# Performance work log

Measured on AMD Instinct MI355X. Metric: run time of the kernel, lower is better.

## Reference

```python
import jax, jax.numpy as jnp
import numpy as np

NEG_INF_DIAG = 1000000.0

def setup_inputs() -> dict:
    key = jax.random.key(0)
    k1, k2, k3 = jax.random.split(key, 3)
    B, N, S, D = 64, 32, 256, 128
    return {
        "query_embeddings": jax.random.normal(k1, (B, N, D), dtype=jnp.float32),
        "doc_embeddings": jax.random.normal(k2, (B, S, D), dtype=jnp.float32),
        "neg_doc_embeddings": jax.random.normal(k3, (B, S, D), dtype=jnp.float32),
    }

def _maxsim(q, d):
    # q: (b, n, dim), d: (b, s, dim) -> (b,) sum over n of max over s of q.d
    return jnp.einsum('bnd,bsd->bns', q, d).max(axis=2).sum(axis=1)

def reference(query_embeddings, doc_embeddings, neg_doc_embeddings):
    pos_scores = _maxsim(query_embeddings, doc_embeddings)
    neg_scores = _maxsim(query_embeddings, neg_doc_embeddings)
    loss = jax.nn.softplus(neg_scores - pos_scores).mean()

    # in-batch term: scores[b, c] = MaxSim(query b, doc c)
    scores = jnp.einsum('bnd,csd->bcns', query_embeddings, doc_embeddings).max(axis=3).sum(axis=2)  # (B, B)
    pos = jnp.diagonal(scores)
    B = scores.shape[0]
    neg = (scores - jnp.eye(B, dtype=scores.dtype) * NEG_INF_DIAG).max(axis=1)
    loss = loss + jax.nn.softplus(neg - pos).mean()
    return loss / 2
```

## Files before the change

### kernel.cpp

```cpp
#include <hip/hip_runtime.h>
#include <hip/hip_bf16.h>

#define B_SZ 64
#define N_Q 32

typedef __attribute__((ext_vector_type(8))) short bf16x8;
typedef __attribute__((ext_vector_type(4))) float f32x4;

static __device__ __forceinline__ unsigned short f2bf(float f) {
    __hip_bfloat16 h = __float2bfloat16(f);
    return *reinterpret_cast<unsigned short*>(&h);
}

static __device__ __forceinline__ bf16x8 cvt_frag(const float* __restrict__ src) {
    float4 a = reinterpret_cast<const float4*>(src)[0];
    float4 b = reinterpret_cast<const float4*>(src)[1];
    union { bf16x8 v; unsigned short u[8]; } t;
    t.u[0] = f2bf(a.x); t.u[1] = f2bf(a.y); t.u[2] = f2bf(a.z); t.u[3] = f2bf(a.w);
    t.u[4] = f2bf(b.x); t.u[5] = f2bf(b.y); t.u[6] = f2bf(b.z); t.u[7] = f2bf(b.w);
    return t.v;
}

#define MFMA(A, Bv, C) __builtin_amdgcn_mfma_f32_16x16x32_bf16(A, Bv, C, 0, 0, 0)

__global__ __launch_bounds__(256) void cvt_permute(const float* __restrict__ q,
                                                   const float* __restrict__ dd,
                                                   const float* __restrict__ nd,
                                                   unsigned short* __restrict__ DP,
                                                   unsigned short* __restrict__ QP) {
    const int blk = blockIdx.x, tid = threadIdx.x;
    if (blk < 2048) {
        const int o = blk * 256 + tid;
        const int doc = o >> 12;
        const int u = o & 4095;
        const int ln = u & 63, nt = (u >> 6) & 3, kk = (u >> 8) & 3, ch = u >> 10;
        const int s  = ch * 64 + nt * 16 + (ln & 15);
        const int k0 = kk * 32 + (ln >> 4) * 8;
        const float* src = ((doc < 64) ? (dd + (size_t)doc * 32768)
                                       : (nd + (size_t)(doc - 64) * 32768)) + s * 128 + k0;
        reinterpret_cast<bf16x8*>(DP)[o] = cvt_frag(src);
    } else {
        const int g = (blk - 2048) * 256 + tid;
        const int b = g >> 9, u = g & 511;
        const int ln = u & 63, mt = (u >> 6) & 1, kk = u >> 7;
        const int n  = mt * 16 + (ln & 15);
        const int k0 = kk * 32 + (ln >> 4) * 8;
        reinterpret_cast<bf16x8*>(QP)[g] = cvt_frag(q + (size_t)b * 4096 + n * 128 + k0);
    }
}

__global__ __launch_bounds__(256, 2) void maxsim_kernel(const unsigned short* __restrict__ QP,
                                                        const unsigned short* __restrict__ DP,
                                                        float* __restrict__ scores) {
    const int wg  = blockIdx.x;
    const int tid = threadIdx.x;
    const int wave = tid >> 6, lane = tid & 63;
    const int l15 = lane & 15;

    __shared__ bf16x8 docB[4096];
    __shared__ float wredN[4][4][8];

    const bf16x8* DP8 = reinterpret_cast<const bf16x8*>(DP);
    const bf16x8* QP8 = reinterpret_cast<const bf16x8*>(QP);

    int c, b;
    bool isNeg;
    if (wg < 1024) { c = wg >> 4; b = (wg & 15) * 4 + wave; isNeg = false; }
    else           { b = wg - 1024; c = b; isNeg = true; }
    const int dcc = isNeg ? (64 + b) : c;

    bf16x8 Af[4][2];
    const bf16x8* qsrc = QP8 + (size_t)b * 512 + lane;
    #pragma unroll
    for (int kk = 0; kk < 4; ++kk) {
        Af[kk][0] = qsrc[kk * 128];
        Af[kk][1] = qsrc[kk * 128 + 64];
    }

    const bf16x8* dsrc = DP8 + (size_t)dcc * 4096 + wave * 1024 + lane;
    #pragma unroll
    for (int f = 0; f < 16; ++f)
        docB[wave * 1024 + f * 64 + lane] = dsrc[f * 64];
    __syncthreads();

    float rmax[2][4];
    #pragma unroll
    for (int mt = 0; mt < 2; ++mt)
        #pragma unroll
        for (int r = 0; r < 4; ++r) rmax[mt][r] = -3.0e38f;

    const int nch = isNeg ? 1 : 4;
    for (int i = 0; i < nch; ++i) {
        const int ch = isNeg ? wave : ((wave + i) & 3);
        f32x4 acc[2][4] = {};
        #pragma unroll
        for (int kk = 0; kk < 4; ++kk) {
            #pragma unroll
            for (int nt = 0; nt < 4; ++nt) {
                bf16x8 Bv = docB[ch * 1024 + kk * 256 + nt * 64 + lane];
                acc[0][nt] = MFMA(Af[kk][0], Bv, acc[0][nt]);
                acc[1][nt] = MFMA(Af[kk][1], Bv, acc[1][nt]);
            }
        }
        #pragma unroll
        for (int mt = 0; mt < 2; ++mt)
            #pragma unroll
            for (int r = 0; r < 4; ++r)
                rmax[mt][r] = fmaxf(rmax[mt][r],
                    fmaxf(fmaxf(acc[mt][0][r], acc[mt][1][r]),
                          fmaxf(acc[mt][2][r], acc[mt][3][r])));
    }

    float part = 0.0f;
    #pragma unroll
    for (int mt = 0; mt < 2; ++mt)
        #pragma unroll
        for (int r = 0; r < 4; ++r) {
            float m = rmax[mt][r];
            m = fmaxf(m, __shfl_xor(m, 1, 64));
            m = fmaxf(m, __shfl_xor(m, 2, 64));
            m = fmaxf(m, __shfl_xor(m, 4, 64));
            m = fmaxf(m, __shfl_xor(m, 8, 64));
            if (isNeg) {
                if (l15 == 0) wredN[wave][lane >> 4][mt * 4 + r] = m;
            } else {
                part += m;
            }
        }
    if (!isNeg) {
        part += __shfl_xor(part, 16, 64);
        part += __shfl_xor(part, 32, 64);
        if (lane == 0) scores[(size_t)b * 65 + c] = part;
    } else {
        __syncthreads();
        if (tid < 32) {
            const int l4v = tid >> 3, slot = tid & 7;
            float m = fmaxf(fmaxf(wredN[0][l4v][slot], wredN[1][l4v][slot]),
                            fmaxf(wredN[2][l4v][slot], wredN[3][l4v][slot]));
            m += __shfl_xor(m, 1, 64);
            m += __shfl_xor(m, 2, 64);
            m += __shfl_xor(m, 4, 64);
            m += __shfl_xor(m, 8, 64);
            m += __shfl_xor(m, 16, 64);
            if (tid == 0) scores[(size_t)b * 65 + 64] = m;
        }
    }
}

static __device__ __forceinline__ float softplusf(float x) {
    return fmaxf(x, 0.0f) + log1pf(expf(-fabsf(x)));
}

__global__ __launch_bounds__(64) void loss_kernel(const float* __restrict__ scores,
                                                  float* __restrict__ out) {
    const int b = threadIdx.x;
    const float* row = scores + b * 65;
    const float pos  = row[b];
    const float negq = row[64];
    float nib = -1e30f;
    #pragma unroll
    for (int c = 0; c < B_SZ; ++c) {
        float v = row[c] - ((c == b) ? 1000000.0f : 0.0f);
        nib = fmaxf(nib, v);
    }
    float t = softplusf(negq - pos) + softplusf(nib - pos);
    t += __shfl_xor(t, 1, 64);
    t += __shfl_xor(t, 2, 64);
    t += __shfl_xor(t, 4, 64);
    t += __shfl_xor(t, 8, 64);
    t += __shfl_xor(t, 16, 64);
    t += __shfl_xor(t, 32, 64);
    if (b == 0) out[0] = t * (0.5f / 64.0f);
}

extern "C" void kernel_launch(void* const* d_in, const int* in_sizes, int n_in,
                              void* d_out, int out_size, void* d_ws, size_t ws_size,
                              hipStream_t stream) {
    const float* q  = (const float*)d_in[0];
    const float* dd = (const float*)d_in[1];
    const float* nd = (const float*)d_in[2];
    float* out = (float*)d_out;

    unsigned short* DP = (unsigned short*)d_ws;
    unsigned short* QP = DP + (size_t)128 * 32768;
    float* scores = (float*)(QP + (size_t)64 * 4096);

    cvt_permute<<<2176, 256, 0, stream>>>(q, dd, nd, DP, QP);

    maxsim_kernel<<<1024 + B_SZ, 256, 0, stream>>>(QP, DP, scores);

    loss_kernel<<<1, 64, 0, stream>>>(scores, out);
}
```

Before: 90.06 us.

## Fuse loss into maxsim via last-block atomic, use direct global-to-LDS loads

Drops the separate loss kernel launch: each maxsim workgroup bumps a global counter after a fence, and the last one to finish computes the softplus loss from the scores matrix. Document tiles are now loaded with global_load_lds so data goes straight into LDS without passing through registers, and the query fragment loads are issued after them. The workgroup-to-(b,c) mapping is also reordered to change which documents adjacent blocks share, for cache locality. This adds a device-wide atomic and fences, and relies on the counter being reset by the preceding conversion kernel.

```diff
diff --git a/kernel.cpp b/kernel.cpp
--- a/kernel.cpp
+++ b/kernel.cpp
@@ -3,6 +3,7 @@
 
 #define B_SZ 64
 #define N_Q 32
+#define TOTAL_WG 1088
 
 typedef __attribute__((ext_vector_type(8))) short bf16x8;
 typedef __attribute__((ext_vector_type(4))) float f32x4;
@@ -23,12 +24,25 @@
 
 #define MFMA(A, Bv, C) __builtin_amdgcn_mfma_f32_16x16x32_bf16(A, Bv, C, 0, 0, 0)
 
+static __device__ __forceinline__ void gload_lds16(const bf16x8* g, bf16x8* l) {
+    __builtin_amdgcn_global_load_lds(
+        (const __attribute__((address_space(1))) void*)g,
+        (__attribute__((address_space(3))) void*)l,
+        16, 0, 0);
+}
+
+static __device__ __forceinline__ float softplusf(float x) {
+    return fmaxf(x, 0.0f) + log1pf(expf(-fabsf(x)));
+}
+
 __global__ __launch_bounds__(256) void cvt_permute(const float* __restrict__ q,
                                                    const float* __restrict__ dd,
                                                    const float* __restrict__ nd,
                                                    unsigned short* __restrict__ DP,
-                                                   unsigned short* __restrict__ QP) {
+                                                   unsigned short* __restrict__ QP,
+                                                   unsigned int* __restrict__ cnt) {
     const int blk = blockIdx.x, tid = threadIdx.x;
+    if (blk == 0 && tid == 0) *cnt = 0u;
     if (blk < 2048) {
         const int o = blk * 256 + tid;
         const int doc = o >> 12;
@@ -51,7 +65,9 @@
 
 __global__ __launch_bounds__(256, 2) void maxsim_kernel(const unsigned short* __restrict__ QP,
                                                         const unsigned short* __restrict__ DP,
-                                                        float* __restrict__ scores) {
+                                                        float* __restrict__ scores,
+                                                        unsigned int* __restrict__ cnt,
+                                                        float* __restrict__ out) {
     const int wg  = blockIdx.x;
     const int tid = threadIdx.x;
     const int wave = tid >> 6, lane = tid & 63;
@@ -59,15 +75,27 @@
 
     __shared__ bf16x8 docB[4096];
     __shared__ float wredN[4][4][8];
+    __shared__ unsigned int lastBlk;
 
     const bf16x8* DP8 = reinterpret_cast<const bf16x8*>(DP);
     const bf16x8* QP8 = reinterpret_cast<const bf16x8*>(QP);
 
     int c, b;
     bool isNeg;
-    if (wg < 1024) { c = wg >> 4; b = (wg & 15) * 4 + wave; isNeg = false; }
-    else           { b = wg - 1024; c = b; isNeg = true; }
+    if (wg < 1024) {
+        const int x = wg & 7, i = wg >> 3;
+        c = x * 8 + (i & 7);
+        b = (i >> 3) * 4 + wave;
+        isNeg = false;
+    } else {
+        b = wg - 1024; c = b; isNeg = true;
+    }
     const int dcc = isNeg ? (64 + b) : c;
+
+    const bf16x8* dsrc = DP8 + (size_t)dcc * 4096 + wave * 1024 + lane;
+    #pragma unroll
+    for (int f = 0; f < 16; ++f)
+        gload_lds16(dsrc + f * 64, &docB[wave * 1024 + f * 64]);
 
     bf16x8 Af[4][2];
     const bf16x8* qsrc = QP8 + (size_t)b * 512 + lane;
@@ -76,11 +104,6 @@
         Af[kk][0] = qsrc[kk * 128];
         Af[kk][1] = qsrc[kk * 128 + 64];
     }
-
-    const bf16x8* dsrc = DP8 + (size_t)dcc * 4096 + wave * 1024 + lane;
-    #pragma unroll
-    for (int f = 0; f < 16; ++f)
-        docB[wave * 1024 + f * 64 + lane] = dsrc[f * 64];
     __syncthreads();
 
     float rmax[2][4];
@@ -145,32 +168,34 @@
             if (tid == 0) scores[(size_t)b * 65 + 64] = m;
         }
     }
-}
-
-static __device__ __forceinline__ float softplusf(float x) {
-    return fmaxf(x, 0.0f) + log1pf(expf(-fabsf(x)));
-}
-
-__global__ __launch_bounds__(64) void loss_kernel(const float* __restrict__ scores,
-                                                  float* __restrict__ out) {
-    const int b = threadIdx.x;
-    const float* row = scores + b * 65;
-    const float pos  = row[b];
-    const float negq = row[64];
-    float nib = -1e30f;
-    #pragma unroll
-    for (int c = 0; c < B_SZ; ++c) {
-        float v = row[c] - ((c == b) ? 1000000.0f : 0.0f);
-        nib = fmaxf(nib, v);
-    }
-    float t = softplusf(negq - pos) + softplusf(nib - pos);
-    t += __shfl_xor(t, 1, 64);
-    t += __shfl_xor(t, 2, 64);
-    t += __shfl_xor(t, 4, 64);
-    t += __shfl_xor(t, 8, 64);
-    t += __shfl_xor(t, 16, 64);
-    t += __shfl_xor(t, 32, 64);
-    if (b == 0) out[0] = t * (0.5f / 64.0f);
+
+    __threadfence();
+    __syncthreads();
+    if (tid == 0) lastBlk = (atomicAdd(cnt, 1u) == TOTAL_WG - 1u) ? 1u : 0u;
+    __syncthreads();
+    if (lastBlk != 0u) {
+        __threadfence();
+        if (tid < 64) {
+            const int bb = tid;
+            const float* row = scores + bb * 65;
+            const float pos  = row[bb];
+            const float negq = row[64];
+            float nib = -1e30f;
+            #pragma unroll
+            for (int cc = 0; cc < B_SZ; ++cc) {
+                float v = row[cc] - ((cc == bb) ? 1000000.0f : 0.0f);
+                nib = fmaxf(nib, v);
+            }
+            float t = softplusf(negq - pos) + softplusf(nib - pos);
+            t += __shfl_xor(t, 1, 64);
+            t += __shfl_xor(t, 2, 64);
+            t += __shfl_xor(t, 4, 64);
+            t += __shfl_xor(t, 8, 64);
+            t += __shfl_xor(t, 16, 64);
+            t += __shfl_xor(t, 32, 64);
+            if (bb == 0) out[0] = t * (0.5f / 64.0f);
+        }
+    }
 }
 
 extern "C" void kernel_launch(void* const* d_in, const int* in_sizes, int n_in,
@@ -184,10 +209,9 @@
     unsigned short* DP = (unsigned short*)d_ws;
     unsigned short* QP = DP + (size_t)128 * 32768;
     float* scores = (float*)(QP + (size_t)64 * 4096);
-
-    cvt_permute<<<2176, 256, 0, stream>>>(q, dd, nd, DP, QP);
-
-    maxsim_kernel<<<1024 + B_SZ, 256, 0, stream>>>(QP, DP, scores);
-
-    loss_kernel<<<1, 64, 0, stream>>>(scores, out);
-}
+    unsigned int* cnt = (unsigned int*)(scores + 65 * 64);
+
+    cvt_permute<<<2176, 256, 0, stream>>>(q, dd, nd, DP, QP, cnt);
+
+    maxsim_kernel<<<TOTAL_WG, 256, 0, stream>>>(QP, DP, scores, cnt, out);
+}
```

Measured after the change: 153.1 us. 1.7x slower.

## Fuse fp32-to-bf16 conversion into maxsim kernel and remap workgroups for L2 reuse

Applied to the files above, without the earlier changes.

Drops the separate cvt_permute kernel and its workspace. The maxsim kernel now reads fp32 query and doc embeddings directly and converts them to bf16 fragments while filling registers and LDS. This removes one kernel launch and the round trip through a bf16 staging buffer. In exchange, each doc is re-read and re-converted by the 16 workgroups that use it. The workgroup-to-(doc, query group) mapping is also changed so that concurrently scheduled groups spread across docs, which may improve cache locality.

```diff
diff --git a/kernel.cpp b/kernel.cpp
--- a/kernel.cpp
+++ b/kernel.cpp
@@ -23,64 +23,49 @@
 
 #define MFMA(A, Bv, C) __builtin_amdgcn_mfma_f32_16x16x32_bf16(A, Bv, C, 0, 0, 0)
 
-__global__ __launch_bounds__(256) void cvt_permute(const float* __restrict__ q,
-                                                   const float* __restrict__ dd,
-                                                   const float* __restrict__ nd,
-                                                   unsigned short* __restrict__ DP,
-                                                   unsigned short* __restrict__ QP) {
-    const int blk = blockIdx.x, tid = threadIdx.x;
-    if (blk < 2048) {
-        const int o = blk * 256 + tid;
-        const int doc = o >> 12;
-        const int u = o & 4095;
-        const int ln = u & 63, nt = (u >> 6) & 3, kk = (u >> 8) & 3, ch = u >> 10;
-        const int s  = ch * 64 + nt * 16 + (ln & 15);
-        const int k0 = kk * 32 + (ln >> 4) * 8;
-        const float* src = ((doc < 64) ? (dd + (size_t)doc * 32768)
-                                       : (nd + (size_t)(doc - 64) * 32768)) + s * 128 + k0;
-        reinterpret_cast<bf16x8*>(DP)[o] = cvt_frag(src);
-    } else {
-        const int g = (blk - 2048) * 256 + tid;
-        const int b = g >> 9, u = g & 511;
-        const int ln = u & 63, mt = (u >> 6) & 1, kk = u >> 7;
-        const int n  = mt * 16 + (ln & 15);
-        const int k0 = kk * 32 + (ln >> 4) * 8;
-        reinterpret_cast<bf16x8*>(QP)[g] = cvt_frag(q + (size_t)b * 4096 + n * 128 + k0);
-    }
-}
-
-__global__ __launch_bounds__(256, 2) void maxsim_kernel(const unsigned short* __restrict__ QP,
-                                                        const unsigned short* __restrict__ DP,
+__global__ __launch_bounds__(256, 2) void maxsim_kernel(const float* __restrict__ q,
+                                                        const float* __restrict__ dd,
+                                                        const float* __restrict__ nd,
                                                         float* __restrict__ scores) {
     const int wg  = blockIdx.x;
     const int tid = threadIdx.x;
     const int wave = tid >> 6, lane = tid & 63;
-    const int l15 = lane & 15;
+    const int l15 = lane & 15, lhi = lane >> 4;
 
     __shared__ bf16x8 docB[4096];
     __shared__ float wredN[4][4][8];
 
-    const bf16x8* DP8 = reinterpret_cast<const bf16x8*>(DP);
-    const bf16x8* QP8 = reinterpret_cast<const bf16x8*>(QP);
-
     int c, b;
     bool isNeg;
-    if (wg < 1024) { c = wg >> 4; b = (wg & 15) * 4 + wave; isNeg = false; }
-    else           { b = wg - 1024; c = b; isNeg = true; }
-    const int dcc = isNeg ? (64 + b) : c;
+    if (wg < 1024) {
+        const int x = wg & 7, i = wg >> 3;
+        c = x * 8 + (i & 7);
+        b = (i >> 3) * 4 + wave;
+        isNeg = false;
+    } else {
+        b = wg - 1024; c = b; isNeg = true;
+    }
+
+    const float* dsrc = (isNeg ? nd + (size_t)b * 32768
+                               : dd + (size_t)c * 32768);
+    #pragma unroll
+    for (int kk = 0; kk < 4; ++kk)
+        #pragma unroll
+        for (int nt = 0; nt < 4; ++nt) {
+            const int s  = wave * 64 + nt * 16 + l15;
+            const int k0 = kk * 32 + lhi * 8;
+            docB[wave * 1024 + kk * 256 + nt * 64 + lane] =
+                cvt_frag(dsrc + (size_t)s * 128 + k0);
+        }
 
     bf16x8 Af[4][2];
-    const bf16x8* qsrc = QP8 + (size_t)b * 512 + lane;
     #pragma unroll
-    for (int kk = 0; kk < 4; ++kk) {
-        Af[kk][0] = qsrc[kk * 128];
-        Af[kk][1] = qsrc[kk * 128 + 64];
-    }
-
-    const bf16x8* dsrc = DP8 + (size_t)dcc * 4096 + wave * 1024 + lane;
-    #pragma unroll
-    for (int f = 0; f < 16; ++f)
-        docB[wave * 1024 + f * 64 + lane] = dsrc[f * 64];
+    for (int kk = 0; kk < 4; ++kk)
+        #pragma unroll
+        for (int mt = 0; mt < 2; ++mt)
+            Af[kk][mt] = cvt_frag(q + (size_t)b * 4096
+                                    + (size_t)(mt * 16 + l15) * 128
+                                    + kk * 32 + lhi * 8);
     __syncthreads();
 
     float rmax[2][4];
@@ -181,13 +166,8 @@
     const float* nd = (const float*)d_in[2];
     float* out = (float*)d_out;
 
-    unsigned short* DP = (unsigned short*)d_ws;
-    unsigned short* QP = DP + (size_t)128 * 32768;
-    float* scores = (float*)(QP + (size_t)64 * 4096);
+    float* scores = (float*)d_ws;
 
-    cvt_permute<<<2176, 256, 0, stream>>>(q, dd, nd, DP, QP);
-
-    maxsim_kernel<<<1024 + B_SZ, 256, 0, stream>>>(QP, DP, scores);
-
+    maxsim_kernel<<<1024 + B_SZ, 256, 0, stream>>>(q, dd, nd, scores);
     loss_kernel<<<1, 64, 0, stream>>>(scores, out);
 }
```

Result: slower. 98.94 us (+9.9%).

## Keep doc chunk in registers per wave and reuse across 8 queries

Applied to the files above, without the earlier changes.

The maxsim kernel stops staging the whole document in LDS. Each wave now holds one 64-row document chunk in registers and loops over 8 queries, which halves the grid and swaps the LDS round-trip for direct global loads. The cross-chunk max is done through a small shared buffer after a single barrier. The conversion kernel is also changed to read its fp32 source contiguously and scatter the permuted bf16 output, rather than gathering strided reads. The cost is more registers per thread, serial per-query work inside each block, and fewer blocks to spread across CUs.

```diff
diff --git a/kernel.cpp b/kernel.cpp
--- a/kernel.cpp
+++ b/kernel.cpp
@@ -2,7 +2,6 @@
 #include <hip/hip_bf16.h>
 
 #define B_SZ 64
-#define N_Q 32
 
 typedef __attribute__((ext_vector_type(8))) short bf16x8;
 typedef __attribute__((ext_vector_type(4))) float f32x4;
@@ -31,14 +30,16 @@
     const int blk = blockIdx.x, tid = threadIdx.x;
     if (blk < 2048) {
         const int o = blk * 256 + tid;
-        const int doc = o >> 12;
-        const int u = o & 4095;
-        const int ln = u & 63, nt = (u >> 6) & 3, kk = (u >> 8) & 3, ch = u >> 10;
-        const int s  = ch * 64 + nt * 16 + (ln & 15);
-        const int k0 = kk * 32 + (ln >> 4) * 8;
+        const int doc = o >> 12, rem = o & 4095;
         const float* src = ((doc < 64) ? (dd + (size_t)doc * 32768)
-                                       : (nd + (size_t)(doc - 64) * 32768)) + s * 128 + k0;
-        reinterpret_cast<bf16x8*>(DP)[o] = cvt_frag(src);
+                                       : (nd + (size_t)(doc - 64) * 32768)) + rem * 8;
+        bf16x8 v = cvt_frag(src);
+        const int s = rem >> 4, k8 = rem & 15;
+        const int lane = (k8 & 3) * 16 + (s & 15);
+        const int idx = doc * 4096 + (s >> 6) * 1024
+                      + (k8 >> 2) * 256
+                      + ((s >> 4) & 3) * 64 + lane;
+        reinterpret_cast<bf16x8*>(DP)[idx] = v;
     } else {
         const int g = (blk - 2048) * 256 + tid;
         const int b = g >> 9, u = g & 511;
@@ -57,93 +58,75 @@
     const int wave = tid >> 6, lane = tid & 63;
     const int l15 = lane & 15;
 
-    __shared__ bf16x8 docB[4096];
-    __shared__ float wredN[4][4][8];
+    __shared__ float wred[8][4][4][8];
 
     const bf16x8* DP8 = reinterpret_cast<const bf16x8*>(DP);
     const bf16x8* QP8 = reinterpret_cast<const bf16x8*>(QP);
 
-    int c, b;
-    bool isNeg;
-    if (wg < 1024) { c = wg >> 4; b = (wg & 15) * 4 + wave; isNeg = false; }
-    else           { b = wg - 1024; c = b; isNeg = true; }
-    const int dcc = isNeg ? (64 + b) : c;
-
-    bf16x8 Af[4][2];
-    const bf16x8* qsrc = QP8 + (size_t)b * 512 + lane;
-    #pragma unroll
-    for (int kk = 0; kk < 4; ++kk) {
-        Af[kk][0] = qsrc[kk * 128];
-        Af[kk][1] = qsrc[kk * 128 + 64];
+    int c, b0, nb, dcc;
+    if (wg < 512) {
+        const int x = wg & 7, i = wg >> 3;
+        c   = x * 8 + (i & 7);
+        b0  = (i >> 3) * 8;
+        nb  = 8;
+        dcc = c;
+    } else {
+        b0 = wg - 512; c = 64; nb = 1; dcc = 64 + b0;
     }
 
+    bf16x8 Bv[4][4];
     const bf16x8* dsrc = DP8 + (size_t)dcc * 4096 + wave * 1024 + lane;
     #pragma unroll
-    for (int f = 0; f < 16; ++f)
-        docB[wave * 1024 + f * 64 + lane] = dsrc[f * 64];
-    __syncthreads();
+    for (int kk = 0; kk < 4; ++kk)
+        #pragma unroll
+        for (int nt = 0; nt < 4; ++nt)
+            Bv[kk][nt] = dsrc[kk * 256 + nt * 64];
 
-    float rmax[2][4];
-    #pragma unroll
-    for (int mt = 0; mt < 2; ++mt)
+    #pragma unroll 2
+    for (int bi = 0; bi < nb; ++bi) {
+        const int b = b0 + bi;
+        bf16x8 Af[4][2];
+        const bf16x8* qsrc = QP8 + (size_t)b * 512 + lane;
         #pragma unroll
-        for (int r = 0; r < 4; ++r) rmax[mt][r] = -3.0e38f;
-
-    const int nch = isNeg ? 1 : 4;
-    for (int i = 0; i < nch; ++i) {
-        const int ch = isNeg ? wave : ((wave + i) & 3);
+        for (int kk = 0; kk < 4; ++kk) {
+            Af[kk][0] = qsrc[kk * 128];
+            Af[kk][1] = qsrc[kk * 128 + 64];
+        }
         f32x4 acc[2][4] = {};
         #pragma unroll
-        for (int kk = 0; kk < 4; ++kk) {
+        for (int kk = 0; kk < 4; ++kk)
             #pragma unroll
             for (int nt = 0; nt < 4; ++nt) {
-                bf16x8 Bv = docB[ch * 1024 + kk * 256 + nt * 64 + lane];
-                acc[0][nt] = MFMA(Af[kk][0], Bv, acc[0][nt]);
-                acc[1][nt] = MFMA(Af[kk][1], Bv, acc[1][nt]);
+                acc[0][nt] = MFMA(Af[kk][0], Bv[kk][nt], acc[0][nt]);
+                acc[1][nt] = MFMA(Af[kk][1], Bv[kk][nt], acc[1][nt]);
             }
-        }
         #pragma unroll
         for (int mt = 0; mt < 2; ++mt)
             #pragma unroll
-            for (int r = 0; r < 4; ++r)
-                rmax[mt][r] = fmaxf(rmax[mt][r],
-                    fmaxf(fmaxf(acc[mt][0][r], acc[mt][1][r]),
-                          fmaxf(acc[mt][2][r], acc[mt][3][r])));
+            for (int r = 0; r < 4; ++r) {
+                float m = fmaxf(fmaxf(acc[mt][0][r], acc[mt][1][r]),
+                                fmaxf(acc[mt][2][r], acc[mt][3][r]));
+                m = fmaxf(m, __shfl_xor(m, 1, 64));
+                m = fmaxf(m, __shfl_xor(m, 2, 64));
+                m = fmaxf(m, __shfl_xor(m, 4, 64));
+                m = fmaxf(m, __shfl_xor(m, 8, 64));
+                if (l15 == 0) wred[bi][wave][lane >> 4][mt * 4 + r] = m;
+            }
     }
+    __syncthreads();
 
-    float part = 0.0f;
-    #pragma unroll
-    for (int mt = 0; mt < 2; ++mt)
-        #pragma unroll
-        for (int r = 0; r < 4; ++r) {
-            float m = rmax[mt][r];
-            m = fmaxf(m, __shfl_xor(m, 1, 64));
-            m = fmaxf(m, __shfl_xor(m, 2, 64));
-            m = fmaxf(m, __shfl_xor(m, 4, 64));
-            m = fmaxf(m, __shfl_xor(m, 8, 64));
-            if (isNeg) {
-                if (l15 == 0) wredN[wave][lane >> 4][mt * 4 + r] = m;
-            } else {
-                part += m;
-            }
-        }
-    if (!isNeg) {
-        part += __shfl_xor(part, 16, 64);
-        part += __shfl_xor(part, 32, 64);
-        if (lane == 0) scores[(size_t)b * 65 + c] = part;
-    } else {
-        __syncthreads();
-        if (tid < 32) {
-            const int l4v = tid >> 3, slot = tid & 7;
-            float m = fmaxf(fmaxf(wredN[0][l4v][slot], wredN[1][l4v][slot]),
-                            fmaxf(wredN[2][l4v][slot], wredN[3][l4v][slot]));
-            m += __shfl_xor(m, 1, 64);
-            m += __shfl_xor(m, 2, 64);
-            m += __shfl_xor(m, 4, 64);
-            m += __shfl_xor(m, 8, 64);
-            m += __shfl_xor(m, 16, 64);
-            if (tid == 0) scores[(size_t)b * 65 + 64] = m;
-        }
+    if (tid < nb * 32) {
+        const int bi = tid >> 5, n = tid & 31;
+        const int slot = (n >> 4) * 4 + (n & 3);
+        const int lhi  = (n >> 2) & 3;
+        float m = fmaxf(fmaxf(wred[bi][0][lhi][slot], wred[bi][1][lhi][slot]),
+                        fmaxf(wred[bi][2][lhi][slot], wred[bi][3][lhi][slot]));
+        m += __shfl_xor(m, 1, 32);
+        m += __shfl_xor(m, 2, 32);
+        m += __shfl_xor(m, 4, 32);
+        m += __shfl_xor(m, 8, 32);
+        m += __shfl_xor(m, 16, 32);
+        if (n == 0) scores[(size_t)(b0 + bi) * 65 + c] = m;
     }
 }
 
@@ -186,8 +169,6 @@
     float* scores = (float*)(QP + (size_t)64 * 4096);
 
     cvt_permute<<<2176, 256, 0, stream>>>(q, dd, nd, DP, QP);
-
-    maxsim_kernel<<<1024 + B_SZ, 256, 0, stream>>>(QP, DP, scores);
-
+    maxsim_kernel<<<512 + B_SZ, 256, 0, stream>>>(QP, DP, scores);
     loss_kernel<<<1, 64, 0, stream>>>(scores, out);
 }
```

New measurement: 92.58 us. +2.8%, slower.
